# Kernel optimization log

Hardware: AMD Instinct MI355X
Metric: run time of the kernel (lower is better)

Reference implementation:

```python
import jax, jax.numpy as jnp
import numpy as np

B, N, IN_DIM, H, K = 2, 256, 128, 8, 64  # batch, nodes, in_dim, heads, out_dim


def setup_inputs() -> dict:
    key = jax.random.key(0)
    k0, k1, k2, k3, k4, k5 = jax.random.split(key, 6)
    s = 1.0 / np.sqrt(IN_DIM)
    return {
        "h": jax.random.normal(k0, (B, N, IN_DIM), jnp.float32),
        "e_att": jax.random.normal(k1, (B, N, N, H, K), jnp.float32),
        "e_value": jax.random.normal(k2, (B, N, N, H, K), jnp.float32),
        "attn_mask": jnp.ones((B, N, N, 1, 1), dtype=bool),
        "Wq": jax.random.normal(k3, (H * K, IN_DIM), jnp.float32) * s,
        "Wk": jax.random.normal(k4, (H * K, IN_DIM), jnp.float32) * s,
        "Wv": jax.random.normal(k5, (H * K, IN_DIM), jnp.float32) * s,
    }


def reference(h, e_att, e_value, attn_mask, Wq, Wk, Wv):
    b, n = h.shape[:2]
    Q = (h @ Wq.T).reshape(b, n, H, K)
    Km = (h @ Wk.T).reshape(b, n, H, K) * (float(K) ** -0.5)  # scaling on K as in source
    V = (h @ Wv.T).reshape(b, n, H, K)
    # QK 'multiplication' -> [b,i,j,h,1]; KE 'addition' -> broadcast-add edge bias [b,i,j,h,k]
    scores = jnp.einsum('bihk,bjhk->bijh', Q, Km)[..., None] + e_att
    scores = scores - 1e24 * (~attn_mask).astype(scores.dtype)
    attn = jax.nn.softmax(scores, axis=2)  # softmax over source nodes j
    # attn_dropout p=0, dropout_lvl='connections' -> multiply by mask.float()
    attn = attn * attn_mask.astype(attn.dtype)
    # VE 'addition', edge_out_dim == out_dim: h = attn @ V + sum_j attn * E_value
    out = jnp.einsum('bijhk,bjhk->bihk', attn, V) + jnp.einsum('bijhk,bijhk->bihk', attn, e_value)
    return out.reshape(b, n, H * K).astype(jnp.float32)
```

## Files before the change

### kernel.cpp

```cpp
#include <hip/hip_runtime.h>
#include <math.h>

#define B_ 2
#define N_ 256
#define IND_ 128
#define H_ 8
#define K_ 64
#define HK_ 512
#define NH_ 2048
#define LOG2E 1.4426950408889634f
#define SLICES 8
#define JS 32
#define PART_OFF 2097152

__global__ __launch_bounds__(256) void proj_kernel(
    const float* __restrict__ h,
    const float* __restrict__ Wq,
    const float* __restrict__ Wk,
    const float* __restrict__ Wv,
    float* __restrict__ Q, float* __restrict__ Km, float* __restrict__ V)
{
    __shared__ float hs[16][132];
    __shared__ float ws_[16][132];
    const int tx = threadIdx.x, ty = threadIdx.y;
    const int tid = ty * 16 + tx;
    const int c0 = blockIdx.x * 16, r0 = blockIdx.y * 16;
    const int m = blockIdx.z;
    const float* W = (m == 0) ? Wq : (m == 1) ? Wk : Wv;
    for (int f = tid; f < 512; f += 256) {
        int row = f >> 5, c4 = (f & 31) << 2;
        *(float4*)&hs[row][c4]  = *(const float4*)&h[(size_t)(r0 + row) * IND_ + c4];
        *(float4*)&ws_[row][c4] = *(const float4*)&W[(size_t)(c0 + row) * IND_ + c4];
    }
    __syncthreads();
    float acc = 0.f;
#pragma unroll
    for (int d = 0; d < IND_; ++d) acc = fmaf(hs[ty][d], ws_[tx][d], acc);
    if (m == 1) acc *= 0.125f;
    float* outp = (m == 0) ? Q : (m == 1) ? Km : V;
    outp[(size_t)(r0 + ty) * HK_ + (c0 + tx)] = acc;
}

__global__ __launch_bounds__(256) void qk_kernel(
    const float* __restrict__ Q,
    const float* __restrict__ Km,
    float* __restrict__ qk_pre)
{
    const int bi = blockIdx.x;
    const int b  = bi >> 8;
    __shared__ float qrow[HK_];
    for (int idx = threadIdx.x; idx < HK_; idx += 256)
        qrow[idx] = Q[(size_t)bi * HK_ + idx];
    __syncthreads();
#pragma unroll
    for (int it = 0; it < 8; ++it) {
        int p = threadIdx.x + it * 256;
        int j = p >> 3, hh = p & 7;
        const float4* k4p = (const float4*)(Km + ((size_t)(b * N_ + j) * HK_ + hh * K_));
        const float4* q4  = (const float4*)(qrow + hh * K_);
        float acc = 0.f;
#pragma unroll
        for (int d = 0; d < K_ / 4; ++d) {
            float4 a = q4[d], bb = k4p[d];
            acc = fmaf(a.x, bb.x, fmaf(a.y, bb.y, fmaf(a.z, bb.z, fmaf(a.w, bb.w, acc))));
        }
        qk_pre[(size_t)bi * NH_ + p] = acc * LOG2E;
    }
}

__global__ __launch_bounds__(256) void attn_part(
    const float* __restrict__ e_att,
    const float* __restrict__ e_value,
    const float* __restrict__ V,
    const float* __restrict__ qk_pre,
    float* __restrict__ part)
{
    const int bid = blockIdx.x;
    const int bi  = bid >> 3;
    const int sl  = bid & 7;
    const int b   = bi >> 8;
    const int j0  = sl * JS;
    const int tid = threadIdx.x;
    const int sg  = tid >> 7;
    const int t   = tid & 127;
    const int hh  = t >> 4;

    __shared__ float  qs[JS * H_];
    __shared__ float4 red[128][2];

    qs[tid] = qk_pre[(size_t)bi * NH_ + j0 * H_ + tid];
    __syncthreads();

    const int jb = j0 + sg * 16;
    const float4* pe = (const float4*)(e_att   + ((size_t)bi * N_ + jb) * HK_) + t;
    const float4* pv = (const float4*)(e_value + ((size_t)bi * N_ + jb) * HK_) + t;
    const float4* pV = (const float4*)(V + ((size_t)b * N_ + jb) * HK_) + t;
    const float*  qp = qs + sg * 16 * H_ + hh;

    float4 l4 = {0.f, 0.f, 0.f, 0.f};
    float4 a4 = {0.f, 0.f, 0.f, 0.f};

#pragma unroll 4
    for (int s = 0; s < 16; ++s) {
        float4 ea = pe[s * 128];
        float4 ev = pv[s * 128];
        float4 vv = pV[s * 128];
        float  q_ = qp[s * H_];
        float p0 = __builtin_amdgcn_exp2f(fmaf(ea.x, LOG2E, q_));
        float p1 = __builtin_amdgcn_exp2f(fmaf(ea.y, LOG2E, q_));
        float p2 = __builtin_amdgcn_exp2f(fmaf(ea.z, LOG2E, q_));
        float p3 = __builtin_amdgcn_exp2f(fmaf(ea.w, LOG2E, q_));
        l4.x += p0; l4.y += p1; l4.z += p2; l4.w += p3;
        a4.x = fmaf(p0, vv.x + ev.x, a4.x);
        a4.y = fmaf(p1, vv.y + ev.y, a4.y);
        a4.z = fmaf(p2, vv.z + ev.z, a4.z);
        a4.w = fmaf(p3, vv.w + ev.w, a4.w);
    }

    if (sg == 1) { red[t][0] = l4; red[t][1] = a4; }
    __syncthreads();
    if (sg == 0) {
        float4 l2 = red[t][0], a2 = red[t][1];
        l4.x += l2.x; l4.y += l2.y; l4.z += l2.z; l4.w += l2.w;
        a4.x += a2.x; a4.y += a2.y; a4.z += a2.z; a4.w += a2.w;
        float* pp = part + ((size_t)bid * 128 + t) * 8;
        *(float4*)pp       = l4;
        *(float4*)(pp + 4) = a4;
    }
}

__global__ __launch_bounds__(128) void attn_combine(
    const float* __restrict__ part,
    float* __restrict__ out)
{
    const int bi = blockIdx.x;
    const int t  = threadIdx.x;
    float4 L = {0.f, 0.f, 0.f, 0.f};
    float4 A = {0.f, 0.f, 0.f, 0.f};
#pragma unroll
    for (int sl = 0; sl < SLICES; ++sl) {
        const float* pp = part + (((size_t)bi * SLICES + sl) * 128 + t) * 8;
        float4 l2 = *(const float4*)pp;
        float4 a2 = *(const float4*)(pp + 4);
        L.x += l2.x; L.y += l2.y; L.z += l2.z; L.w += l2.w;
        A.x += a2.x; A.y += a2.y; A.z += a2.z; A.w += a2.w;
    }
    float4 res;
    res.x = (L.x > 0.f) ? A.x / L.x : 0.f;
    res.y = (L.y > 0.f) ? A.y / L.y : 0.f;
    res.z = (L.z > 0.f) ? A.z / L.z : 0.f;
    res.w = (L.w > 0.f) ? A.w / L.w : 0.f;
    *(float4*)(out + (size_t)bi * HK_ + t * 4) = res;
}

extern "C" void kernel_launch(void* const* d_in, const int* in_sizes, int n_in,
                              void* d_out, int out_size, void* d_ws, size_t ws_size,
                              hipStream_t stream)
{
    const float* h     = (const float*)d_in[0];
    const float* e_att = (const float*)d_in[1];
    const float* e_val = (const float*)d_in[2];
    const float* Wq = (const float*)d_in[4];
    const float* Wk = (const float*)d_in[5];
    const float* Wv = (const float*)d_in[6];
    float* out = (float*)d_out;

    float* ws = (float*)d_ws;
    float* Q  = ws;
    float* Km = ws + 262144;
    float* V  = ws + 524288;
    float* qk = ws + 786432;
    float* part = ws + PART_OFF;

    hipLaunchKernelGGL(proj_kernel, dim3(32, 32, 3), dim3(16, 16), 0, stream,
                       h, Wq, Wk, Wv, Q, Km, V);
    hipLaunchKernelGGL(qk_kernel, dim3(512), dim3(256), 0, stream, Q, Km, qk);
    hipLaunchKernelGGL(attn_part, dim3(B_ * N_ * SLICES), dim3(256), 0, stream,
                       e_att, e_val, V, qk, part);
    hipLaunchKernelGGL(attn_combine, dim3(B_ * N_), dim3(128), 0, stream,
                       part, out);
}
```

Before: 171.8 us.

## Stream edge tensors through LDS with triple-buffered async global_load_lds pipeline

Rewrites the attention partial kernel so each block covers 64 source nodes (4 slices instead of 8). e_att, e_value and V tiles are copied straight into shared memory with global_load_lds DMA, using three rotating slots and explicit vmcnt waits so loads overlap compute. The goal is to keep more memory requests in flight on this bandwidth-bound kernel. In exchange it uses about 72KB of LDS per block, which lowers occupancy, and it adds two barriers per batch.

```diff
diff --git a/kernel.cpp b/kernel.cpp
--- a/kernel.cpp
+++ b/kernel.cpp
@@ -9,8 +9,9 @@
 #define HK_ 512
 #define NH_ 2048
 #define LOG2E 1.4426950408889634f
-#define SLICES 8
-#define JS 32
+#define SLICES 4
+#define JS 64
+#define NBATCH 16
 #define PART_OFF 2097152
 
 __global__ __launch_bounds__(256) void proj_kernel(
@@ -68,6 +69,13 @@
     }
 }
 
+__device__ __forceinline__ void dma16(const float* g, float* l) {
+    __builtin_amdgcn_global_load_lds(
+        (const __attribute__((address_space(1))) unsigned int*)g,
+        (__attribute__((address_space(3))) unsigned int*)l,
+        16, 0, 0);
+}
+
 __global__ __launch_bounds__(256) void attn_part(
     const float* __restrict__ e_att,
     const float* __restrict__ e_value,
@@ -76,54 +84,87 @@
     float* __restrict__ part)
 {
     const int bid = blockIdx.x;
-    const int bi  = bid >> 3;
-    const int sl  = bid & 7;
+    const int bi  = bid >> 2;
+    const int sl  = bid & 3;
     const int b   = bi >> 8;
     const int j0  = sl * JS;
     const int tid = threadIdx.x;
-    const int sg  = tid >> 7;
-    const int t   = tid & 127;
-    const int hh  = t >> 4;
-
-    __shared__ float  qs[JS * H_];
+    const int wv  = tid >> 6;
+    const int lane = tid & 63;
+    const int f   = tid & 127;
+    const int jp  = tid >> 7;
+    const int hh  = f >> 4;
+
+    __shared__ float slots[3 * 6144];
+    __shared__ float qs[JS * H_];
     __shared__ float4 red[128][2];
 
-    qs[tid] = qk_pre[(size_t)bi * NH_ + j0 * H_ + tid];
-    __syncthreads();
-
-    const int jb = j0 + sg * 16;
-    const float4* pe = (const float4*)(e_att   + ((size_t)bi * N_ + jb) * HK_) + t;
-    const float4* pv = (const float4*)(e_value + ((size_t)bi * N_ + jb) * HK_) + t;
-    const float4* pV = (const float4*)(V + ((size_t)b * N_ + jb) * HK_) + t;
-    const float*  qp = qs + sg * 16 * H_ + hh;
+    qs[tid]       = qk_pre[(size_t)bi * NH_ + j0 * H_ + tid];
+    qs[tid + 256] = qk_pre[(size_t)bi * NH_ + j0 * H_ + tid + 256];
+
+    const float* ea_b = e_att   + ((size_t)bi * N_ + j0) * HK_;
+    const float* ev_b = e_value + ((size_t)bi * N_ + j0) * HK_;
+    const float* v_b  = V + ((size_t)b * N_ + j0) * HK_;
+
+#define ISSUE(bt, slotf) { \
+    const int jb_ = (bt) * 4; \
+    _Pragma("unroll") for (int q = 0; q < 6; ++q) { \
+        int u  = wv + q * 4; \
+        int tt = u >> 3, r = u & 7, jj = r >> 1, hf = r & 1; \
+        const float* base = (tt == 0) ? ea_b : (tt == 1) ? ev_b : v_b; \
+        const float* src = base + (size_t)(jb_ + jj) * HK_ + hf * 256 + lane * 4; \
+        dma16(src, (slotf) + u * 256); \
+    } }
+
+#define COMPUTE(bt, sb) { \
+    _Pragma("unroll") for (int jj2 = 0; jj2 < 2; ++jj2) { \
+        int jj = jp * 2 + jj2; \
+        float4 ea = *(const float4*)((sb) + jj * 512 + f * 4); \
+        float4 ev = *(const float4*)((sb) + 2048 + jj * 512 + f * 4); \
+        float4 vv = *(const float4*)((sb) + 4096 + jj * 512 + f * 4); \
+        float  q_ = qs[((bt) * 4 + jj) * 8 + hh]; \
+        float p0 = __builtin_amdgcn_exp2f(fmaf(ea.x, LOG2E, q_)); \
+        float p1 = __builtin_amdgcn_exp2f(fmaf(ea.y, LOG2E, q_)); \
+        float p2 = __builtin_amdgcn_exp2f(fmaf(ea.z, LOG2E, q_)); \
+        float p3 = __builtin_amdgcn_exp2f(fmaf(ea.w, LOG2E, q_)); \
+        l4.x += p0; l4.y += p1; l4.z += p2; l4.w += p3; \
+        a4.x = fmaf(p0, vv.x + ev.x, a4.x); \
+        a4.y = fmaf(p1, vv.y + ev.y, a4.y); \
+        a4.z = fmaf(p2, vv.z + ev.z, a4.z); \
+        a4.w = fmaf(p3, vv.w + ev.w, a4.w); \
+    } }
+
+#define ITER(bt, WN) { \
+    asm volatile("s_waitcnt vmcnt(" #WN ")" ::: "memory"); \
+    __syncthreads(); \
+    const float* sb_ = slots + ((bt) % 3) * 6144; \
+    COMPUTE(bt, sb_); \
+    __syncthreads(); \
+    if ((bt) + 3 < NBATCH) ISSUE((bt) + 3, slots + (((bt) + 3) % 3) * 6144); \
+    }
 
     float4 l4 = {0.f, 0.f, 0.f, 0.f};
     float4 a4 = {0.f, 0.f, 0.f, 0.f};
 
-#pragma unroll 4
-    for (int s = 0; s < 16; ++s) {
-        float4 ea = pe[s * 128];
-        float4 ev = pv[s * 128];
-        float4 vv = pV[s * 128];
-        float  q_ = qp[s * H_];
-        float p0 = __builtin_amdgcn_exp2f(fmaf(ea.x, LOG2E, q_));
-        float p1 = __builtin_amdgcn_exp2f(fmaf(ea.y, LOG2E, q_));
-        float p2 = __builtin_amdgcn_exp2f(fmaf(ea.z, LOG2E, q_));
-        float p3 = __builtin_amdgcn_exp2f(fmaf(ea.w, LOG2E, q_));
-        l4.x += p0; l4.y += p1; l4.z += p2; l4.w += p3;
-        a4.x = fmaf(p0, vv.x + ev.x, a4.x);
-        a4.y = fmaf(p1, vv.y + ev.y, a4.y);
-        a4.z = fmaf(p2, vv.z + ev.z, a4.z);
-        a4.w = fmaf(p3, vv.w + ev.w, a4.w);
-    }
-
-    if (sg == 1) { red[t][0] = l4; red[t][1] = a4; }
+    ISSUE(0, slots)
+    ISSUE(1, slots + 6144)
+    ISSUE(2, slots + 12288)
+
+    ITER(0, 12)  ITER(1, 12)  ITER(2, 12)  ITER(3, 12)
+    ITER(4, 12)  ITER(5, 12)  ITER(6, 12)  ITER(7, 12)
+    ITER(8, 12)  ITER(9, 12)  ITER(10, 12) ITER(11, 12)
+    ITER(12, 12) ITER(13, 12) ITER(14, 6)  ITER(15, 0)
+#undef ITER
+#undef COMPUTE
+#undef ISSUE
+
+    if (jp == 1) { red[f][0] = l4; red[f][1] = a4; }
     __syncthreads();
-    if (sg == 0) {
-        float4 l2 = red[t][0], a2 = red[t][1];
+    if (jp == 0) {
+        float4 l2 = red[f][0], a2 = red[f][1];
         l4.x += l2.x; l4.y += l2.y; l4.z += l2.z; l4.w += l2.w;
         a4.x += a2.x; a4.y += a2.y; a4.z += a2.z; a4.w += a2.w;
-        float* pp = part + ((size_t)bid * 128 + t) * 8;
+        float* pp = part + ((size_t)bid * 128 + f) * 8;
         *(float4*)pp       = l4;
         *(float4*)(pp + 4) = a4;
     }
```

New measurement: 169.7 us. No clear change (-1.2%).
